# Kernel tuning notes

Measured on AMD Instinct MI355X. Metric: run time of the kernel, lower is better.

The kernel has to match this reference:

```python
import jax, jax.numpy as jnp
import numpy as np

COUNT, L1, L2, L3 = 8, 3072, 15, 32


def setup_inputs() -> dict:
    key = jax.random.key(0)
    ks = jax.random.split(key, 10)
    B = 16384
    x = jax.random.uniform(ks[0], (B, L1), dtype=jnp.float32)
    ls_indices = jax.random.randint(ks[1], (B,), 0, COUNT, dtype=jnp.int32)
    s = 1.0 / np.sqrt(L1)
    l1_w = jax.random.uniform(ks[2], (COUNT * (L2 + 1), L1), minval=-s, maxval=s, dtype=jnp.float32)
    l1_b = jax.random.uniform(ks[3], (COUNT * (L2 + 1),), minval=-s, maxval=s, dtype=jnp.float32)
    # l1_fact initialized to zero in the module; use small random values for a
    # meaningful numeric test (same math either way)
    l1f_w = 0.01 * jax.random.normal(ks[4], (L2 + 1, L1), dtype=jnp.float32)
    l1f_b = 0.01 * jax.random.normal(ks[5], (L2 + 1,), dtype=jnp.float32)
    s2 = 1.0 / np.sqrt(2 * L2)
    l2_w = jax.random.uniform(ks[6], (COUNT * L3, 2 * L2), minval=-s2, maxval=s2, dtype=jnp.float32)
    l2_b = jax.random.uniform(ks[7], (COUNT * L3,), minval=-s2, maxval=s2, dtype=jnp.float32)
    s3 = 1.0 / np.sqrt(L3)
    out_w = jax.random.uniform(ks[8], (COUNT, L3), minval=-s3, maxval=s3, dtype=jnp.float32)
    out_b = jnp.zeros((COUNT,), dtype=jnp.float32)
    return {"x": x, "ls_indices": ls_indices, "l1_w": l1_w, "l1_b": l1_b,
            "l1f_w": l1f_w, "l1f_b": l1f_b, "l2_w": l2_w, "l2_b": l2_b,
            "out_w": out_w, "out_b": out_b}


def _gather_bucket(dense, idx):
    # dense: [B, count, F]; idx: [B] -> [B, F]
    return jnp.take_along_axis(dense, idx[:, None, None], axis=1)[:, 0, :]


def reference(x, ls_indices, l1_w, l1_b, l1f_w, l1f_b, l2_w, l2_b, out_w, out_b):
    B = x.shape[0]
    idx = ls_indices.reshape(-1)
    # L1 stage: dense over all buckets, then gather selected bucket
    l1s = (x @ l1_w.T + l1_b).reshape(B, COUNT, L2 + 1)
    l1c = _gather_bucket(l1s, idx)                      # [B, L2+1]
    l1f = x @ l1f_w.T + l1f_b                           # [B, L2+1]
    l1c_main, l1c_out = l1c[:, :L2], l1c[:, L2:]
    l1f_main, l1f_out = l1f[:, :L2], l1f[:, L2:]
    l1x = l1c_main + l1f_main
    # squared-clipped-ReLU pair: [x^2 * 127/128, x] clamped to [0,1]
    l1x = jnp.clip(jnp.concatenate([jnp.square(l1x) * (127.0 / 128.0), l1x], axis=1), 0.0, 1.0)
    # L2 stage
    l2s = (l1x @ l2_w.T + l2_b).reshape(B, COUNT, L3)
    l2x = jnp.clip(_gather_bucket(l2s, idx), 0.0, 1.0)  # [B, L3]
    # output stage
    l3s = (l2x @ out_w.T + out_b).reshape(B, COUNT, 1)
    l3c = _gather_bucket(l3s, idx)                      # [B, 1]
    return l3c + l1f_out + l1c_out
```

## Files before the change

kernel.cpp:

```cpp
#include <hip/hip_runtime.h>
#include <stdint.h>

#define L1D 3072
#define NB 16384
#define CAP 4096
#define CHUNKS 80

typedef float  float4v  __attribute__((ext_vector_type(4)));
typedef short  short8   __attribute__((ext_vector_type(8)));

__device__ __forceinline__ unsigned short f2bf(float f) {
  uint32_t u = __builtin_bit_cast(uint32_t, f);
  u += 0x7fffu + ((u >> 16) & 1u);
  return (unsigned short)(u >> 16);
}

__device__ __forceinline__ void gload_lds16(const void* g, void* l) {
  __builtin_amdgcn_global_load_lds((const __attribute__((address_space(1))) unsigned int*)g,
                                   (__attribute__((address_space(3))) unsigned int*)l, 16, 0, 0);
}

__global__ void prep_kernel(const float* __restrict__ l1w, const float* __restrict__ l1b,
                            const float* __restrict__ l1fw, const float* __restrict__ l1fb,
                            unsigned short* __restrict__ cw, float* __restrict__ cb,
                            int* __restrict__ cur) {
  const int n = blockIdx.y;
  const int k = blockIdx.x * 256 + threadIdx.x;
  const unsigned short v = f2bf(l1w[n * L1D + k] + l1fw[(n & 15) * L1D + k]);
  const int kk  = k >> 5;
  const int sub = (k >> 3) & 3;
  const int e   = k & 7;
  const int lane = sub * 16 + (n & 15);
  cw[(((n >> 4) * 96 + kk) * 64 + lane) * 8 + e] = v;
  if (blockIdx.x == 0 && n == 0 && threadIdx.x < 128)
    cb[threadIdx.x] = l1b[threadIdx.x] + l1fb[threadIdx.x & 15];
  if (blockIdx.x == 0 && n == 0 && threadIdx.x < 8) cur[threadIdx.x] = 0;
}

__global__ void scatter_kernel(const int* __restrict__ lsi, int* __restrict__ cur,
                               int* __restrict__ sorted) {
  __shared__ int hist[8], base[8];
  const int tid = threadIdx.x;
  if (tid < 8) hist[tid] = 0;
  __syncthreads();
  const int i = blockIdx.x * 256 + tid;
  const int b = lsi[i];
  const int slot = atomicAdd(&hist[b], 1);
  __syncthreads();
  if (tid < 8) base[tid] = atomicAdd(&cur[tid], hist[tid]);
  __syncthreads();
  sorted[b * CAP + base[b] + slot] = i;
}

struct __align__(16) EpS {
  float ygp[2][32][20];
  float l2wb[960];
  float outwb[32];
  float l2bb[32];
  float biasb[16];
  int   rows[32];
};

union __align__(16) SMem {
  struct { char slab[4][2][6144]; } st;
  EpS ep;
};

__global__ __launch_bounds__(256, 3) void fused_kernel(
    const float* __restrict__ x, const unsigned short* __restrict__ cw,
    const float* __restrict__ cb,
    const float* __restrict__ gl2w, const float* __restrict__ gl2b,
    const float* __restrict__ goutw, const float* __restrict__ goutb,
    const int* __restrict__ cur, const int* __restrict__ sorted,
    float* __restrict__ out) {
  __shared__ SMem sm;
  const int tid  = threadIdx.x;
  const int lane = tid & 63;
  const int wid  = tid >> 6;
  const int bucket = blockIdx.x & 7;
  const int chunk  = blockIdx.x >> 3;
  const int count  = cur[bucket];
  const int start  = chunk * 32;
  if (start >= count) return;

  const int h = wid >> 1;
  const int p = wid & 1;

  const char* aP[4];
#pragma unroll
  for (int q = 0; q < 4; ++q) {
    const int lr = q * 4 + (lane >> 4);
    int sr = start + h * 16 + lr;
    sr = (sr < count) ? sr : (count - 1);
    const int grow = sorted[bucket * CAP + sr];
    const int co = ((lane & 15) * 16) ^ ((lr & 7) << 4);
    aP[q] = (const char*)x + (size_t)grow * (L1D * 4) + p * 6144 + co;
  }
  const char* bP = (const char*)cw + ((size_t)bucket * 96 * 64 + lane) * 16
                 + (size_t)p * 48 * 1024;
  char* slab = (char*)sm.st.slab[wid];

  float4v acc = {0.f, 0.f, 0.f, 0.f};

#define STAGE(BUF_, IDX_)                                                       \
  {                                                                             \
    char* d_ = slab + (BUF_) * 6144;                                            \
    _Pragma("unroll")                                                           \
    for (int q = 0; q < 4; ++q)                                                 \
      gload_lds16(aP[q] + (IDX_) * 256, d_ + q * 1024);                         \
    _Pragma("unroll")                                                           \
    for (int ks = 0; ks < 2; ++ks)                                              \
      gload_lds16(bP + (size_t)((IDX_) * 2 + ks) * 1024, d_ + 4096 + ks * 1024);\
  }

#define BODY(BUF_, DOSTAGE_, NIDX_)                                             \
  {                                                                             \
    const char* base_ = slab + (BUF_) * 6144;                                   \
    const int r_ = lane & 15, sw_ = (r_ & 7) << 4;                              \
    short8 afr[2], bfr[2];                                                      \
    _Pragma("unroll")                                                           \
    for (int ks = 0; ks < 2; ++ks) {                                            \
      const int G_ = ks * 128 + (lane >> 4) * 32;                               \
      const float4v lo = *(const float4v*)(base_ + r_ * 256 + (G_ ^ sw_));      \
      const float4v hi = *(const float4v*)(base_ + r_ * 256 + ((G_ + 16) ^ sw_));\
      afr[ks] = short8{(short)f2bf(lo.x), (short)f2bf(lo.y), (short)f2bf(lo.z), \
                       (short)f2bf(lo.w), (short)f2bf(hi.x), (short)f2bf(hi.y), \
                       (short)f2bf(hi.z), (short)f2bf(hi.w)};                   \
      bfr[ks] = *(const short8*)(base_ + 4096 + ks * 1024 + lane * 16);         \
    }                                                                           \
    asm volatile("" ::: "memory");       \
    if (DOSTAGE_) STAGE(BUF_, NIDX_)                                            \
    _Pragma("unroll")                                                           \
    for (int ks = 0; ks < 2; ++ks)                                              \
      acc = __builtin_amdgcn_mfma_f32_16x16x32_bf16(afr[ks], bfr[ks], acc, 0, 0, 0); \
  }

  STAGE(0, 0)
  STAGE(1, 1)

#pragma unroll 2
  for (int idx = 0; idx < 22; ++idx) {
    asm volatile("s_waitcnt vmcnt(6)" ::: "memory");
    BODY(idx & 1, 1, idx + 2)
  }
  asm volatile("s_waitcnt vmcnt(6)" ::: "memory");
  BODY(0, 0, 0)
  asm volatile("s_waitcnt vmcnt(0)" ::: "memory");
  BODY(1, 0, 0)
#undef STAGE
#undef BODY

  __syncthreads();

  if (tid < 32) {
    const int sr = start + tid;
    sm.ep.rows[tid]  = (sr < count) ? sorted[bucket * CAP + sr] : -1;
    sm.ep.outwb[tid] = goutw[bucket * 32 + tid];
    sm.ep.l2bb[tid]  = gl2b[bucket * 32 + tid];
  }
  if (tid < 16) sm.ep.biasb[tid] = cb[bucket * 16 + tid];
  for (int i = tid; i < 960; i += 256) sm.ep.l2wb[i] = gl2w[bucket * 960 + i];
#pragma unroll
  for (int rg = 0; rg < 4; ++rg)
    sm.ep.ygp[p][h * 16 + (lane >> 4) * 4 + rg][lane & 15] = acc[rg];
  __syncthreads();

  {
    const int r = tid >> 3, q = tid & 7;
    const int grow = sm.ep.rows[r];
    float act[30];
#pragma unroll
    for (int c = 0; c < 15; ++c) {
      const float v = sm.ep.ygp[0][r][c] + sm.ep.ygp[1][r][c] + sm.ep.biasb[c];
      act[c]      = fminf(v * v * (127.0f / 128.0f), 1.0f);
      act[15 + c] = fminf(fmaxf(v, 0.0f), 1.0f);
    }
    const float y15 = sm.ep.ygp[0][r][15] + sm.ep.ygp[1][r][15] + sm.ep.biasb[15];
    float o = 0.0f;
#pragma unroll
    for (int nn = 0; nn < 4; ++nn) {
      const int n = q * 4 + nn;
      float s = sm.ep.l2bb[n];
#pragma unroll
      for (int k = 0; k < 30; ++k) s += act[k] * sm.ep.l2wb[n * 30 + k];
      s = fminf(fmaxf(s, 0.0f), 1.0f);
      o += s * sm.ep.outwb[n];
    }
    o += __shfl_down(o, 4, 8);
    o += __shfl_down(o, 2, 8);
    o += __shfl_down(o, 1, 8);
    if (q == 0 && grow >= 0) out[grow] = o + y15 + goutb[bucket];
  }
}

extern "C" void kernel_launch(void* const* d_in, const int* in_sizes, int n_in,
                              void* d_out, int out_size, void* d_ws, size_t ws_size,
                              hipStream_t stream) {
  const float* x    = (const float*)d_in[0];
  const int*   lsi  = (const int*)d_in[1];
  const float* l1w  = (const float*)d_in[2];
  const float* l1b  = (const float*)d_in[3];
  const float* l1fw = (const float*)d_in[4];
  const float* l1fb = (const float*)d_in[5];
  const float* l2w  = (const float*)d_in[6];
  const float* l2b  = (const float*)d_in[7];
  const float* outw = (const float*)d_in[8];
  const float* outb = (const float*)d_in[9];
  float* out = (float*)d_out;

  unsigned short* cw = (unsigned short*)d_ws;
  float* cb   = (float*)((char*)d_ws + 786432);
  int*   cur  = (int*)  ((char*)d_ws + 786944);
  int*   sorted = (int*)((char*)d_ws + 786976);

  prep_kernel<<<dim3(12, 128), 256, 0, stream>>>(l1w, l1b, l1fw, l1fb, cw, cb, cur);
  scatter_kernel<<<NB / 256, 256, 0, stream>>>(lsi, cur, sorted);
  fused_kernel<<<8 * CHUNKS, 256, 0, stream>>>(x, cw, cb, l2w, l2b, outw, outb,
                                               cur, sorted, out);
}
```

Before: 303.0 us.

## Shrink row tile to 16 and split K across waves with shared LDS staging

Each block now handles 16 rows instead of 32. The four waves share one double-buffered A/B tile in LDS, and each wave computes a different K slice of every 1024-element step; the partials are reduced across waves in the epilogue. This gives more blocks (152 chunks per bucket) to spread across CUs and cuts per-block register and LDS footprint. In exchange it adds block-wide barriers every iteration and fewer MFMAs per byte of staged weights, and it rereads the weight tile from global memory twice as often.

```diff
diff --git a/kernel.cpp b/kernel.cpp
--- a/kernel.cpp
+++ b/kernel.cpp
@@ -4,7 +4,9 @@
 #define L1D 3072
 #define NB 16384
 #define CAP 4096
-#define CHUNKS 80
+#define ROWS 16
+#define CHUNKS 152
+#define TITER 12
 
 typedef float  float4v  __attribute__((ext_vector_type(4)));
 typedef short  short8   __attribute__((ext_vector_type(8)));
@@ -53,16 +55,19 @@
 }
 
 struct __align__(16) EpS {
-  float ygp[2][32][20];
+  float ygp[4][ROWS][20];
   float l2wb[960];
   float outwb[32];
   float l2bb[32];
   float biasb[16];
-  int   rows[32];
+  int   rows[ROWS];
 };
 
 union __align__(16) SMem {
-  struct { char slab[4][2][6144]; } st;
+  struct {
+    float Af[2][ROWS][256];
+    unsigned short Bf[2][8][512];
+  } st;
   EpS ep;
 };
 
@@ -80,102 +85,104 @@
   const int bucket = blockIdx.x & 7;
   const int chunk  = blockIdx.x >> 3;
   const int count  = cur[bucket];
-  const int start  = chunk * 32;
+  const int start  = chunk * ROWS;
   if (start >= count) return;
 
-  const int h = wid >> 1;
-  const int p = wid & 1;
-
   const char* aP[4];
 #pragma unroll
   for (int q = 0; q < 4; ++q) {
-    const int lr = q * 4 + (lane >> 4);
-    int sr = start + h * 16 + lr;
+    const int br = wid * 4 + q;
+    int sr = start + br;
     sr = (sr < count) ? sr : (count - 1);
     const int grow = sorted[bucket * CAP + sr];
-    const int co = ((lane & 15) * 16) ^ ((lr & 7) << 4);
-    aP[q] = (const char*)x + (size_t)grow * (L1D * 4) + p * 6144 + co;
-  }
-  const char* bP = (const char*)cw + ((size_t)bucket * 96 * 64 + lane) * 16
-                 + (size_t)p * 48 * 1024;
-  char* slab = (char*)sm.st.slab[wid];
+    aP[q] = (const char*)x + (size_t)grow * (L1D * 4) + (size_t)(lane ^ (br & 7)) * 16;
+  }
+  const char* bP = (const char*)cw + ((size_t)bucket * 96 * 64 + lane) * 16;
 
   float4v acc = {0.f, 0.f, 0.f, 0.f};
 
-#define STAGE(BUF_, IDX_)                                                       \
-  {                                                                             \
-    char* d_ = slab + (BUF_) * 6144;                                            \
-    _Pragma("unroll")                                                           \
-    for (int q = 0; q < 4; ++q)                                                 \
-      gload_lds16(aP[q] + (IDX_) * 256, d_ + q * 1024);                         \
-    _Pragma("unroll")                                                           \
-    for (int ks = 0; ks < 2; ++ks)                                              \
-      gload_lds16(bP + (size_t)((IDX_) * 2 + ks) * 1024, d_ + 4096 + ks * 1024);\
-  }
-
-#define BODY(BUF_, DOSTAGE_, NIDX_)                                             \
-  {                                                                             \
-    const char* base_ = slab + (BUF_) * 6144;                                   \
-    const int r_ = lane & 15, sw_ = (r_ & 7) << 4;                              \
-    short8 afr[2], bfr[2];                                                      \
-    _Pragma("unroll")                                                           \
-    for (int ks = 0; ks < 2; ++ks) {                                            \
-      const int G_ = ks * 128 + (lane >> 4) * 32;                               \
-      const float4v lo = *(const float4v*)(base_ + r_ * 256 + (G_ ^ sw_));      \
-      const float4v hi = *(const float4v*)(base_ + r_ * 256 + ((G_ + 16) ^ sw_));\
-      afr[ks] = short8{(short)f2bf(lo.x), (short)f2bf(lo.y), (short)f2bf(lo.z), \
-                       (short)f2bf(lo.w), (short)f2bf(hi.x), (short)f2bf(hi.y), \
-                       (short)f2bf(hi.z), (short)f2bf(hi.w)};                   \
-      bfr[ks] = *(const short8*)(base_ + 4096 + ks * 1024 + lane * 16);         \
-    }                                                                           \
-    asm volatile("" ::: "memory");       \
-    if (DOSTAGE_) STAGE(BUF_, NIDX_)                                            \
-    _Pragma("unroll")                                                           \
-    for (int ks = 0; ks < 2; ++ks)                                              \
-      acc = __builtin_amdgcn_mfma_f32_16x16x32_bf16(afr[ks], bfr[ks], acc, 0, 0, 0); \
+#define STAGE(BUF_, T_)                                                          \
+  {                                                                              \
+    _Pragma("unroll")                                                            \
+    for (int q = 0; q < 4; ++q)                                                  \
+      gload_lds16(aP[q] + (size_t)(T_) * 1024, &sm.st.Af[BUF_][wid * 4 + q][0]); \
+    _Pragma("unroll")                                                            \
+    for (int j = 0; j < 2; ++j)                                                  \
+      gload_lds16(bP + (size_t)((T_) * 8 + wid * 2 + j) * 1024,                  \
+                  &sm.st.Bf[BUF_][wid * 2 + j][0]);                              \
+  }
+
+#define COMPUTE(BUF_)                                                            \
+  {                                                                              \
+    const int r_ = lane & 15, s_ = (r_ & 7);                                     \
+    _Pragma("unroll")                                                            \
+    for (int kq = 0; kq < 2; ++kq) {                                             \
+      const int ks = wid * 2 + kq;                                               \
+      const int c1 = (ks * 128 + (lane >> 4) * 32) >> 4;      \
+      const float4v lo = *(const float4v*)((const char*)&sm.st.Af[BUF_][r_][0]   \
+                                           + ((c1 ^ s_) << 4));                  \
+      const float4v hi = *(const float4v*)((const char*)&sm.st.Af[BUF_][r_][0]   \
+                                           + (((c1 + 1) ^ s_) << 4));            \
+      const short8 afr = short8{(short)f2bf(lo.x), (short)f2bf(lo.y),            \
+                                (short)f2bf(lo.z), (short)f2bf(lo.w),            \
+                                (short)f2bf(hi.x), (short)f2bf(hi.y),            \
+                                (short)f2bf(hi.z), (short)f2bf(hi.w)};           \
+      const short8 bfr = *(const short8*)&sm.st.Bf[BUF_][ks][lane * 8];          \
+      acc = __builtin_amdgcn_mfma_f32_16x16x32_bf16(afr, bfr, acc, 0, 0, 0);     \
+    }                                                                            \
   }
 
   STAGE(0, 0)
   STAGE(1, 1)
-
-#pragma unroll 2
-  for (int idx = 0; idx < 22; ++idx) {
-    asm volatile("s_waitcnt vmcnt(6)" ::: "memory");
-    BODY(idx & 1, 1, idx + 2)
-  }
   asm volatile("s_waitcnt vmcnt(6)" ::: "memory");
-  BODY(0, 0, 0)
-  asm volatile("s_waitcnt vmcnt(0)" ::: "memory");
-  BODY(1, 0, 0)
+  __builtin_amdgcn_s_barrier();
+
+#pragma unroll 1
+  for (int t = 0; t < TITER; ++t) {
+    COMPUTE(t & 1)
+    asm volatile("" ::: "memory");
+    __builtin_amdgcn_s_barrier();
+    if (t + 2 < TITER) {
+      STAGE(t & 1, t + 2)
+      asm volatile("s_waitcnt vmcnt(6)" ::: "memory");
+    } else {
+      asm volatile("s_waitcnt vmcnt(0)" ::: "memory");
+    }
+    __builtin_amdgcn_s_barrier();
+  }
 #undef STAGE
-#undef BODY
-
-  __syncthreads();
-
+#undef COMPUTE
+
+  __syncthreads();
+
+  if (tid < ROWS) {
+    const int sr = start + tid;
+    sm.ep.rows[tid] = (sr < count) ? sorted[bucket * CAP + sr] : -1;
+  }
   if (tid < 32) {
-    const int sr = start + tid;
-    sm.ep.rows[tid]  = (sr < count) ? sorted[bucket * CAP + sr] : -1;
     sm.ep.outwb[tid] = goutw[bucket * 32 + tid];
     sm.ep.l2bb[tid]  = gl2b[bucket * 32 + tid];
   }
-  if (tid < 16) sm.ep.biasb[tid] = cb[bucket * 16 + tid];
+  if (tid >= 32 && tid < 48) sm.ep.biasb[tid - 32] = cb[bucket * 16 + (tid - 32)];
   for (int i = tid; i < 960; i += 256) sm.ep.l2wb[i] = gl2w[bucket * 960 + i];
 #pragma unroll
   for (int rg = 0; rg < 4; ++rg)
-    sm.ep.ygp[p][h * 16 + (lane >> 4) * 4 + rg][lane & 15] = acc[rg];
-  __syncthreads();
-
-  {
+    sm.ep.ygp[wid][(lane >> 4) * 4 + rg][lane & 15] = acc[rg];
+  __syncthreads();
+
+  if (tid < ROWS * 8) {
     const int r = tid >> 3, q = tid & 7;
     const int grow = sm.ep.rows[r];
     float act[30];
 #pragma unroll
     for (int c = 0; c < 15; ++c) {
-      const float v = sm.ep.ygp[0][r][c] + sm.ep.ygp[1][r][c] + sm.ep.biasb[c];
+      const float v = sm.ep.ygp[0][r][c] + sm.ep.ygp[1][r][c] +
+                      sm.ep.ygp[2][r][c] + sm.ep.ygp[3][r][c] + sm.ep.biasb[c];
       act[c]      = fminf(v * v * (127.0f / 128.0f), 1.0f);
       act[15 + c] = fminf(fmaxf(v, 0.0f), 1.0f);
     }
-    const float y15 = sm.ep.ygp[0][r][15] + sm.ep.ygp[1][r][15] + sm.ep.biasb[15];
+    const float y15 = sm.ep.ygp[0][r][15] + sm.ep.ygp[1][r][15] +
+                      sm.ep.ygp[2][r][15] + sm.ep.ygp[3][r][15] + sm.ep.biasb[15];
     float o = 0.0f;
 #pragma unroll
     for (int nn = 0; nn < 4; ++nn) {
```

After: 299.1 us. No clear change (-1.3%).
